# Kernel optimization log

Measured on AMD Instinct MI355X. Metric: run time of the kernel, lower is better.

## Reference

```python
import jax, jax.numpy as jnp
import numpy as np

B, H, L, DM = 16, 8, 512, 512
DK = DM // H  # 64
POW = 2


def setup_inputs() -> dict:
    rng = jax.random.key(0)
    ks = jax.random.split(rng, 16)
    s = 0.05
    d = {
        "query": jax.random.normal(ks[0], (B, L, DM), jnp.float32),
        "key": jax.random.normal(ks[1], (B, L, DM), jnp.float32),
        "value": jax.random.normal(ks[2], (B, L, DM), jnp.float32),
        # torch nn.Linear weights: [out_features, in_features]
        "Wq": jax.random.normal(ks[3], (DM, DM), jnp.float32) * s,
        "bq": jax.random.normal(ks[4], (DM,), jnp.float32) * s,
        "Wk": jax.random.normal(ks[5], (DM, DM), jnp.float32) * s,
        "bk": jax.random.normal(ks[6], (DM,), jnp.float32) * s,
        "Wv": jax.random.normal(ks[7], (DM, DM), jnp.float32) * s,
        "bv": jax.random.normal(ks[8], (DM,), jnp.float32) * s,
        # FCgamma: d_k -> 2 (LrMo == 2)
        "Wg": jax.random.normal(ks[9], (2, DK), jnp.float32) * s,
        "bg": jnp.full((2,), 0.05, jnp.float32),
        "lam1": jnp.zeros((1,), jnp.float32),
        "Wo": jax.random.normal(ks[10], (DM, DM), jnp.float32) * s,
        "bo": jax.random.normal(ks[11], (DM,), jnp.float32) * s,
    }
    return d


def reference(query, key, value, Wq, bq, Wk, bk, Wv, bv, Wg, bg, lam1, Wo, bo):
    def proj(x, W, b):
        # (B,L,DM) -> (B,H,L,DK)
        return (x @ W.T + b).reshape(B, L, H, DK).transpose(0, 2, 1, 3)

    q = proj(query, Wq, bq)
    k = proj(key, Wk, bk)
    v = proj(value, Wv, bv)

    # NOTE: original code overwrites the scaled scores with unscaled QK^T
    scores = jnp.einsum('bhqd,bhkd->bhqk', q, k)  # [B,H,L,L]
    attn = jax.nn.softmax(scores, axis=-1)

    # LrMo == 2: per-row gammas from FCgamma(q) -> 2 channels
    g = q @ Wg.T + bg                      # [B,H,L,2]
    qp = (jnp.abs(g) + 1.0) ** (-POW)      # (|g|+1)^(-pow)

    t = jnp.arange(L, dtype=jnp.float32)
    dist = -0.5 * (t[:, None] - t[None, :]) ** 2   # dist[i,j] = -(i-j)^2/2
    tril = jnp.tril(dist, -1)
    triu = jnp.triu(dist, 0)
    # diag_embed(v) @ M == row-scaling v[i]*M[i,:]
    adj = jnp.exp(qp[..., 1][..., None] * tril + qp[..., 0][..., None] * triu)

    # max-normalize rows of attn
    attn = attn / jnp.max(attn, axis=-1, keepdims=True)
    # sigmoid-gated mix with distance adjacency
    sg = jax.nn.sigmoid(lam1)  # shape (1,)
    attn = sg * attn + (1.0 - sg) * adj
    # degree (row-sum) normalization, non-symmetric
    attn = attn / (jnp.sum(attn, axis=-1, keepdims=True) + 1e-9)

    out = jnp.einsum('bhqk,bhkd->bhqd', attn, v)
    out = out.transpose(0, 2, 1, 3).reshape(B, L, DM)
    return out @ Wo.T + bo
```

## Files before the change

### kernel.cpp

```cpp
#include <hip/hip_runtime.h>
#include <hip/hip_fp16.h>
#include <math.h>

#define B_  16
#define H_  8
#define L_  512
#define DM_ 512
#define DK_ 64
#define LOG2E_ 1.44269504088896340736f
#define NLOG2E_H_ 0.72134752044f

typedef _Float16 f16;
typedef __attribute__((ext_vector_type(2)))  __fp16   fp16v2;
typedef __attribute__((ext_vector_type(8)))  _Float16 f16x8;
typedef __attribute__((ext_vector_type(16))) float f32x16;

__device__ __forceinline__ unsigned pkrtz(float a, float b) {
    union { fp16v2 v; unsigned u; } cv;
    cv.v = __builtin_amdgcn_cvt_pkrtz(a, b);
    return cv.u;
}
__device__ __forceinline__ void plswap(unsigned &x, unsigned &y) {
    asm("v_permlane32_swap_b32 %0, %1" : "+v"(x), "+v"(y));
}

__global__ __launch_bounds__(256) void convw_pack(
    const float* __restrict__ Wq, const float* __restrict__ Wk,
    const float* __restrict__ Wv, const float* __restrict__ Wo,
    f16* __restrict__ Wpk)
{
    const float* src[4] = {Wq, Wk, Wv, Wo};
    const int t = blockIdx.x * 256 + threadIdx.x;
    const int m    = t >> 15;
    const int r    = t & 32767;
    const int lane = r & 31;
    const int hf   = (r >> 5) & 1;
    const int ks   = (r >> 6) & 31;
    const int nb   = r >> 11;
    const float* p = src[m] + (size_t)(nb * 32 + lane) * 512 + ks * 16 + hf * 8;
    float4 x0 = *(const float4*)(p);
    float4 x1 = *(const float4*)(p + 4);
    uint4 v;
    v.x = pkrtz(x0.x, x0.y); v.y = pkrtz(x0.z, x0.w);
    v.z = pkrtz(x1.x, x1.y); v.w = pkrtz(x1.z, x1.w);
    *(uint4*)&Wpk[(size_t)m * 262144 + (size_t)r * 8] = v;
}

template<int XF16, int OUTF32, int OUTMODE, int NWAVES, int NT>
__device__ __forceinline__ void gemm_stream_core(
    const void* __restrict__ Xv, const f16* __restrict__ Wpk_m,
    const float* __restrict__ bias, void* __restrict__ Yv,
    int row0, int col0, f16* Xl)
{
    const int tid   = threadIdx.x;
    const int w     = tid >> 6;
    const int lane  = tid & 63;
    const int lq    = lane & 31;
    const int half_ = lane >> 5;
    const int colw  = col0 + w * (NT * 32);

    {
        constexpr int TPR = NWAVES * 64 / 32;
        constexpr int FPT = 512 / TPR;
        const int r = tid / TPR, s = tid % TPR;
        const unsigned swz = (r & 7) << 4;
        if (XF16) {
            const f16* X = (const f16*)Xv + (size_t)(row0 + r) * 512 + s * FPT;
            #pragma unroll
            for (int j = 0; j < FPT / 8; ++j) {
                uint4 v = *(const uint4*)(X + j * 8);
                *(uint4*)((char*)Xl + ((r * 1024 + s * FPT * 2 + j * 16) ^ swz)) = v;
            }
        } else {
            const float* X = (const float*)Xv + (size_t)(row0 + r) * 512 + s * FPT;
            #pragma unroll
            for (int j = 0; j < FPT / 8; ++j) {
                float4 x0 = *(const float4*)(X + j * 8);
                float4 x1 = *(const float4*)(X + j * 8 + 4);
                uint4 v;
                v.x = pkrtz(x0.x, x0.y); v.y = pkrtz(x0.z, x0.w);
                v.z = pkrtz(x1.x, x1.y); v.w = pkrtz(x1.z, x1.w);
                *(uint4*)((char*)Xl + ((r * 1024 + s * FPT * 2 + j * 16) ^ swz)) = v;
            }
        }
    }
    __syncthreads();

    f32x16 acc[NT];
    #pragma unroll
    for (int nt = 0; nt < NT; ++nt)
        #pragma unroll
        for (int i = 0; i < 16; ++i) acc[nt][i] = 0.f;

    const f16* wp[NT];
    #pragma unroll
    for (int nt = 0; nt < NT; ++nt)
        wp[nt] = Wpk_m + ((size_t)((colw / 32 + nt) * 64 + half_)) * 256 + lq * 8;

    const unsigned aswz = (lq & 7) << 4;

    #pragma unroll 4
    for (int ks = 0; ks < 32; ++ks) {
        f16x8 a = *(const f16x8*)((char*)Xl + ((lq * 1024 + ks * 32 + half_ * 16) ^ aswz));
        f16x8 bfr[NT];
        #pragma unroll
        for (int nt = 0; nt < NT; ++nt)
            bfr[nt] = *(const f16x8*)(wp[nt] + (size_t)ks * 512);
        #pragma unroll
        for (int nt = 0; nt < NT; ++nt) {
            if (OUTMODE == 2)
                acc[nt] = __builtin_amdgcn_mfma_f32_32x32x16_f16(bfr[nt], a, acc[nt], 0, 0, 0);
            else
                acc[nt] = __builtin_amdgcn_mfma_f32_32x32x16_f16(a, bfr[nt], acc[nt], 0, 0, 0);
        }
    }

    if (OUTMODE == 2) {
        const int b  = row0 >> 9;
        const int cb = (row0 >> 5) & 15;
        f16* Kp = (f16*)Yv + (size_t)(b * H_ + w) * 32768;
        #pragma unroll
        for (int nt = 0; nt < NT; ++nt)
            #pragma unroll
            for (int g = 0; g < 4; ++g) {
                const int n0 = w * 64 + nt * 32 + 8 * g + 4 * half_;
                const float4 b4 = *(const float4*)&bias[n0];
                const int ks2 = nt * 2 + (g >> 1);
                uint2 v;
                v.x = pkrtz(acc[nt][4 * g + 0] + b4.x, acc[nt][4 * g + 1] + b4.y);
                v.y = pkrtz(acc[nt][4 * g + 2] + b4.z, acc[nt][4 * g + 3] + b4.w);
                *(uint2*)&Kp[(cb * 4 + ks2) * 512 + (g & 1) * 256 + lq * 8 + half_ * 4] = v;
            }
    } else if (OUTMODE == 1) {
        const int b  = row0 >> 9;
        const int cB = row0 & 511;
        const int tt = cB >> 6;
        const int kbase = (cB >> 4) & 3;
        f16* Vp = (f16*)Yv + (size_t)(b * H_ + w) * 32768;
        #pragma unroll
        for (int nt = 0; nt < NT; ++nt) {
            const float bv = bias[w * 64 + nt * 32 + lq];
            #pragma unroll
            for (int g = 0; g < 4; ++g) {
                const int ks2 = kbase + (g >> 1);
                uint2 v;
                v.x = pkrtz(acc[nt][4 * g + 0] + bv, acc[nt][4 * g + 1] + bv);
                v.y = pkrtz(acc[nt][4 * g + 2] + bv, acc[nt][4 * g + 3] + bv);
                *(uint2*)&Vp[((tt * 4 + ks2) * 2 + nt) * 512 + (g & 1) * 256 + lq * 8 + half_ * 4] = v;
            }
        }
    } else {
        #pragma unroll
        for (int nt = 0; nt < NT; ++nt) {
            const float bv = bias[colw + nt * 32 + lq];
            #pragma unroll
            for (int r = 0; r < 16; ++r) {
                const int row = row0 + (r & 3) + 8 * (r >> 2) + 4 * half_;
                const float v = acc[nt][r] + bv;
                const size_t off = (size_t)row * 512 + colw + nt * 32 + lq;
                if (OUTF32) ((float*)Yv)[off] = v;
                else        ((f16*)Yv)[off]   = (f16)v;
            }
        }
    }
}

__global__ __launch_bounds__(512) void gemm_qkv(
    const float* __restrict__ query, const float* __restrict__ key,
    const float* __restrict__ value, const f16* __restrict__ Wpk,
    const float* __restrict__ bq, const float* __restrict__ bk,
    const float* __restrict__ bv,
    void* __restrict__ Qb, void* __restrict__ Kpk, void* __restrict__ Vpk)
{
    __shared__ f16 Xl[32 * 512];
    const int wg  = blockIdx.x;
    const int xcd = wg & 7;
    const int i   = wg >> 3;
    const int pg  = xcd * 96 + i;
    const int z   = pg >> 8;
    const int y   = pg & 255;
    const int row0 = y * 32;

    if (z == 0)
        gemm_stream_core<0, 0, 0, 8, 2>(query, Wpk,          bq, Qb,  row0, 0, Xl);
    else if (z == 1)
        gemm_stream_core<0, 0, 2, 8, 2>(key,   Wpk + 262144, bk, Kpk, row0, 0, Xl);
    else
        gemm_stream_core<0, 0, 1, 8, 2>(value, Wpk + 524288, bv, Vpk, row0, 0, Xl);
}

__global__ __launch_bounds__(256) void gemm_o(
    const void* __restrict__ X, const f16* __restrict__ Wpk,
    const float* __restrict__ bo, void* __restrict__ Y)
{
    __shared__ f16 Xl[32 * 512];
    const int wg  = blockIdx.x;
    const int xcd = wg & 7;
    const int i   = wg >> 3;
    const int pg  = xcd * 64 + i;
    const int cb  = pg & 1;
    const int y   = pg >> 1;
    gemm_stream_core<1, 1, 0, 4, 2>(X, Wpk + 786432, bo, Y, y * 32, cb * 256, Xl);
}

__global__ __launch_bounds__(256) void attn_kernel(
    const f16* __restrict__ Q, const f16* __restrict__ Kpk,
    const f16* __restrict__ Vpk, const float* __restrict__ Wg,
    const float* __restrict__ bg, const float* __restrict__ lam1,
    f16* __restrict__ ATT)
{
    const int tid  = threadIdx.x;
    const int w    = tid >> 6;
    const int lane = tid & 63;
    const int lq   = lane & 31;
    const int half = lane >> 5;
    const int bh   = blockIdx.x;
    const int b    = bh >> 3;
    const int h    = bh & 7;
    const int q0w  = blockIdx.y * 128 + w * 32;
    const int q    = q0w + lq;

    const float sg  = 1.f / (1.f + __expf(-lam1[0]));
    const float osg = 1.f - sg;

    f16x8 qh[4];
    {
        const f16* qrow = Q + ((size_t)(b * L_ + q) * DM_ + h * DK_);
        #pragma unroll
        for (int db = 0; db < 4; ++db)
            qh[db] = *(const f16x8*)&qrow[db * 16 + 8 * half];
    }

    float A0, A1, qpw;
    {
        float g0 = 0.f, g1 = 0.f;
        #pragma unroll
        for (int db = 0; db < 4; ++db)
            #pragma unroll
            for (int j = 0; j < 8; ++j) {
                const int d = db * 16 + 8 * half + j;
                const float qv = (float)qh[db][j];
                g0 = fmaf(qv, Wg[d], g0);
                g1 = fmaf(qv, Wg[64 + d], g1);
            }
        g0 += __shfl_xor(g0, 32);
        g1 += __shfl_xor(g1, 32);
        g0 += bg[0];
        g1 += bg[1];
        const float t0 = fabsf(g0) + 1.f, t1 = fabsf(g1) + 1.f;
        const float p0 = 1.f / (t0 * t0), p1 = 1.f / (t1 * t1);
        A0 = -NLOG2E_H_ * p0;
        A1 = -NLOG2E_H_ * p1;
        float mn = NLOG2E_H_ * fminf(p0, p1);
        #pragma unroll
        for (int off = 1; off < 64; off <<= 1) mn = fminf(mn, __shfl_xor(mn, off));
        qpw = mn;
    }

    f32x16 aS0, aS1, aA0, aA1;
    #pragma unroll
    for (int i = 0; i < 16; ++i) { aS0[i] = 0.f; aS1[i] = 0.f; aA0[i] = 0.f; aA1[i] = 0.f; }
    float m2 = -3.0e38f, sumS = 0.f, sumA = 0.f;

    const f16* Kp = Kpk + (size_t)(b * H_ + h) * 32768;
    const f16* Vp = Vpk + (size_t)(b * H_ + h) * 32768;
    const int  fo = half * 256 + lq * 8;

    for (int t = 0; t < 8; ++t) {
        const int c0 = t * 64;

        f16x8 ka[4], kb2[4];
        #pragma unroll
        for (int db = 0; db < 4; ++db) {
            ka[db]  = *(const f16x8*)&Kp[(t * 2 * 4 + db) * 512 + fo];
            kb2[db] = *(const f16x8*)&Kp[((t * 2 + 1) * 4 + db) * 512 + fo];
        }

        f32x16 s2a, s2b;
        #pragma unroll
        for (int i = 0; i < 16; ++i) { s2a[i] = 0.f; s2b[i] = 0.f; }
        __builtin_amdgcn_s_setprio(1);
        #pragma unroll
        for (int db = 0; db < 4; ++db) {
            s2a = __builtin_amdgcn_mfma_f32_32x32x16_f16(ka[db],  qh[db], s2a, 0, 0, 0);
            s2b = __builtin_amdgcn_mfma_f32_32x32x16_f16(kb2[db], qh[db], s2b, 0, 0, 0);
        }
        __builtin_amdgcn_s_setprio(0);

        f16x8 vfa[4], vfb[4];
        #pragma unroll
        for (int ks = 0; ks < 4; ++ks) {
            vfa[ks] = *(const f16x8*)&Vp[((t * 4 + ks) * 2 + 0) * 512 + fo];
            vfb[ks] = *(const f16x8*)&Vp[((t * 4 + ks) * 2 + 1) * 512 + fo];
        }

        float tm = s2a[0];
        #pragma unroll
        for (int i = 1; i < 16; ++i) tm = fmaxf(tm, s2a[i]);
        #pragma unroll
        for (int i = 0; i < 16; ++i) tm = fmaxf(tm, s2b[i]);
        tm = fmaxf(tm, __shfl_xor(tm, 32));
        if (__any(tm > m2)) {
            const float nm = fmaxf(m2, tm);
            const float sc = exp2f((m2 - nm) * LOG2E_);
            m2 = nm;
            sumS *= sc;
            #pragma unroll
            for (int r = 0; r < 16; ++r) {
                const float s_ = __shfl(sc, (r & 3) + 8 * (r >> 2) + 4 * half);
                aS0[r] *= s_;
                aS1[r] *= s_;
            }
        }

        const float nmL = m2 * LOG2E_;
        #pragma unroll
        for (int sub = 0; sub < 2; ++sub) {
            const f32x16& s2 = sub ? s2b : s2a;
            #pragma unroll
            for (int ksl = 0; ksl < 2; ++ksl) {
                const int rb = ksl * 8;
                float p[8];
                #pragma unroll
                for (int rr = 0; rr < 8; ++rr) {
                    p[rr] = exp2f(fmaf(s2[rb + rr], LOG2E_, -nmL));
                    sumS += p[rr];
                }
                union { unsigned u[4]; f16x8 v; } f;
                f.u[0] = pkrtz(p[0], p[1]);
                f.u[1] = pkrtz(p[2], p[3]);
                f.u[2] = pkrtz(p[4], p[5]);
                f.u[3] = pkrtz(p[6], p[7]);
                plswap(f.u[0], f.u[2]);
                plswap(f.u[1], f.u[3]);
                const int ks = sub * 2 + ksl;
                __builtin_amdgcn_s_setprio(1);
                aS0 = __builtin_amdgcn_mfma_f32_32x32x16_f16(f.v, vfa[ks], aS0, 0, 0, 0);
                aS1 = __builtin_amdgcn_mfma_f32_32x32x16_f16(f.v, vfb[ks], aS1, 0, 0, 0);
                __builtin_amdgcn_s_setprio(0);
            }
        }

        int gl_ = q0w - (c0 + 63);
        int gh_ = c0 - (q0w + 31);
        int dmin = gl_ > gh_ ? gl_ : gh_;
        if (dmin < 0) dmin = 0;
        if (qpw * (float)(dmin * dmin) < 40.0f) {
            #pragma unroll
            for (int sub = 0; sub < 2; ++sub) {
                #pragma unroll
                for (int ksl = 0; ksl < 2; ++ksl) {
                    float a[8];
                    #pragma unroll
                    for (int rr = 0; rr < 8; ++rr) {
                        const int kk = (rr & 3) + 8 * (rr >> 2) + 16 * ksl + 4 * half;
                        const int diff = q - (c0 + sub * 32 + kk);
                        const float fd = (float)diff;
                        const float coef = diff > 0 ? A1 : A0;
                        a[rr] = exp2f(coef * fd * fd);
                        sumA += a[rr];
                    }
                    union { unsigned u[4]; f16x8 v; } f;
                    f.u[0] = pkrtz(a[0], a[1]);
                    f.u[1] = pkrtz(a[2], a[3]);
                    f.u[2] = pkrtz(a[4], a[5]);
                    f.u[3] = pkrtz(a[6], a[7]);
                    plswap(f.u[0], f.u[2]);
                    plswap(f.u[1], f.u[3]);
                    const int ks = sub * 2 + ksl;
                    __builtin_amdgcn_s_setprio(1);
                    aA0 = __builtin_amdgcn_mfma_f32_32x32x16_f16(f.v, vfa[ks], aA0, 0, 0, 0);
                    aA1 = __builtin_amdgcn_mfma_f32_32x32x16_f16(f.v, vfb[ks], aA1, 0, 0, 0);
                    __builtin_amdgcn_s_setprio(0);
                }
            }
        }
    }

    const float St = sumS + __shfl_xor(sumS, 32);
    const float At = sumA + __shfl_xor(sumA, 32);
    const float den = sg * St + osg * At + 1e-9f;
    #pragma unroll
    for (int r = 0; r < 16; ++r) {
        const int row = (r & 3) + 8 * (r >> 2) + 4 * half;
        const float dn = __shfl(den, row);
        const float o0 = (sg * aS0[r] + osg * aA0[r]) / dn;
        const float o1 = (sg * aS1[r] + osg * aA1[r]) / dn;
        const size_t base = (size_t)(b * L_ + q0w + row) * DM_ + h * DK_;
        ATT[base + lq]      = (f16)o0;
        ATT[base + 32 + lq] = (f16)o1;
    }
}

extern "C" void kernel_launch(void* const* d_in, const int* in_sizes, int n_in,
                              void* d_out, int out_size, void* d_ws, size_t ws_size,
                              hipStream_t stream)
{
    (void)in_sizes; (void)n_in; (void)out_size; (void)ws_size;
    const float* query = (const float*)d_in[0];
    const float* key   = (const float*)d_in[1];
    const float* value = (const float*)d_in[2];
    const float* Wq = (const float*)d_in[3];  const float* bq = (const float*)d_in[4];
    const float* Wk = (const float*)d_in[5];  const float* bk = (const float*)d_in[6];
    const float* Wv = (const float*)d_in[7];  const float* bv = (const float*)d_in[8];
    const float* Wg = (const float*)d_in[9];  const float* bg = (const float*)d_in[10];
    const float* lam1 = (const float*)d_in[11];
    const float* Wo = (const float*)d_in[12]; const float* bo = (const float*)d_in[13];

    f16* ws16 = (f16*)d_ws;
    const size_t NR = (size_t)B_ * L_ * DM_;
    f16* Kpkb = ws16;
    f16* Vpkb = ws16 + NR;
    f16* Qb   = ws16 + 2 * NR;
    f16* Wpkb = ws16 + 3 * NR;
    f16* ATTb = Qb;

    convw_pack<<<512, 256, 0, stream>>>(Wq, Wk, Wv, Wo, Wpkb);

    gemm_qkv<<<768, 512, 0, stream>>>(query, key, value, Wpkb, bq, bk, bv,
                                      Qb, Kpkb, Vpkb);

    dim3 ga(H_ * B_, L_ / 128);
    attn_kernel<<<ga, 256, 0, stream>>>(Qb, Kpkb, Vpkb, Wg, bg, lam1, ATTb);

    gemm_o<<<512, 256, 0, stream>>>(Qb, Wpkb, bo, (float*)d_out);
}
```

Before: 75.32 us.

## Split key range across wave pairs in attention with LDS merge

Each workgroup now handles 64 query rows instead of 128, with two waves per 32-row query tile, each processing half of the key blocks. Partial softmax max, sums and accumulators from the second wave are written to shared memory and merged flash-decoding style by the first wave before normalization. This doubles the grid to raise occupancy and parallelism, at the cost of duplicated Q/gamma setup, about 32KB of LDS and a block barrier.

```diff
diff --git a/kernel.cpp b/kernel.cpp
--- a/kernel.cpp
+++ b/kernel.cpp
@@ -209,15 +209,20 @@
     const float* __restrict__ bg, const float* __restrict__ lam1,
     f16* __restrict__ ATT)
 {
+    __shared__ float Lm[2][64], Lss[2][64], Lsa[2][64];
+    __shared__ float Lacc[2][4][16][64];
+
     const int tid  = threadIdx.x;
     const int w    = tid >> 6;
+    const int pr   = w >> 1;
+    const int ws   = w & 1;
     const int lane = tid & 63;
     const int lq   = lane & 31;
     const int half = lane >> 5;
     const int bh   = blockIdx.x;
     const int b    = bh >> 3;
     const int h    = bh & 7;
-    const int q0w  = blockIdx.y * 128 + w * 32;
+    const int q0w  = blockIdx.y * 64 + pr * 32;
     const int q    = q0w + lq;
 
     const float sg  = 1.f / (1.f + __expf(-lam1[0]));
@@ -266,7 +271,8 @@
     const f16* Vp = Vpk + (size_t)(b * H_ + h) * 32768;
     const int  fo = half * 256 + lq * 8;
 
-    for (int t = 0; t < 8; ++t) {
+    for (int tt = 0; tt < 4; ++tt) {
+        const int t  = ws * 4 + tt;
         const int c0 = t * 64;
 
         f16x8 ka[4], kb2[4];
@@ -377,18 +383,43 @@
         }
     }
 
-    const float St = sumS + __shfl_xor(sumS, 32);
-    const float At = sumA + __shfl_xor(sumA, 32);
-    const float den = sg * St + osg * At + 1e-9f;
-    #pragma unroll
-    for (int r = 0; r < 16; ++r) {
-        const int row = (r & 3) + 8 * (r >> 2) + 4 * half;
-        const float dn = __shfl(den, row);
-        const float o0 = (sg * aS0[r] + osg * aA0[r]) / dn;
-        const float o1 = (sg * aS1[r] + osg * aA1[r]) / dn;
-        const size_t base = (size_t)(b * L_ + q0w + row) * DM_ + h * DK_;
-        ATT[base + lq]      = (f16)o0;
-        ATT[base + 32 + lq] = (f16)o1;
+    if (ws == 1) {
+        Lm[pr][lane]  = m2;
+        Lss[pr][lane] = sumS;
+        Lsa[pr][lane] = sumA;
+        #pragma unroll
+        for (int r = 0; r < 16; ++r) {
+            Lacc[pr][0][r][lane] = aS0[r];
+            Lacc[pr][1][r][lane] = aS1[r];
+            Lacc[pr][2][r][lane] = aA0[r];
+            Lacc[pr][3][r][lane] = aA1[r];
+        }
+    }
+    __syncthreads();
+    if (ws == 0) {
+        const float m2p = Lm[pr][lane];
+        const float nm  = fmaxf(m2, m2p);
+        const float e0  = exp2f((m2  - nm) * LOG2E_);
+        const float e1  = exp2f((m2p - nm) * LOG2E_);
+        const float ssm = sumS * e0 + Lss[pr][lane] * e1;
+        const float sam = sumA + Lsa[pr][lane];
+        const float St  = ssm + __shfl_xor(ssm, 32);
+        const float At  = sam + __shfl_xor(sam, 32);
+        const float den = sg * St + osg * At + 1e-9f;
+        #pragma unroll
+        for (int r = 0; r < 16; ++r) {
+            const int row = (r & 3) + 8 * (r >> 2) + 4 * half;
+            const float dn  = __shfl(den, row);
+            const float e0r = __shfl(e0, row);
+            const float e1r = __shfl(e1, row);
+            const float o0 = (sg * (aS0[r] * e0r + Lacc[pr][0][r][lane] * e1r)
+                            + osg * (aA0[r] + Lacc[pr][2][r][lane])) / dn;
+            const float o1 = (sg * (aS1[r] * e0r + Lacc[pr][1][r][lane] * e1r)
+                            + osg * (aA1[r] + Lacc[pr][3][r][lane])) / dn;
+            const size_t base = (size_t)(b * L_ + q0w + row) * DM_ + h * DK_;
+            ATT[base + lq]      = (f16)o0;
+            ATT[base + 32 + lq] = (f16)o1;
+        }
     }
 }
 
@@ -420,7 +451,7 @@
     gemm_qkv<<<768, 512, 0, stream>>>(query, key, value, Wpkb, bq, bk, bv,
                                       Qb, Kpkb, Vpkb);
 
-    dim3 ga(H_ * B_, L_ / 128);
+    dim3 ga(H_ * B_, L_ / 64);
     attn_kernel<<<ga, 256, 0, stream>>>(Qb, Kpkb, Vpkb, Wg, bg, lam1, ATTb);
 
     gemm_o<<<512, 256, 0, stream>>>(Qb, Wpkb, bo, (float*)d_out);
```

Result: slower. 84.13 us (+11.7%).
